# Kernel optimization log

Measured on AMD Instinct MI355X. Metric: run time of the kernel, lower is better.

## Reference

```python
import jax, jax.numpy as jnp
import numpy as np

OMEGA = 30.0
B = 65536
NUM_FREQ = 8  # int(base_dim / in_features) = 32 / 4


def _siren_w(k, out_dim, in_dim, first=False):
    bound = (1.0 / in_dim) if first else (np.sqrt(6.0 / in_dim) / OMEGA)
    return jax.random.uniform(k, (out_dim, in_dim), jnp.float32, -bound, bound)


def _lin_w(k, out_dim, in_dim):
    bound = np.sqrt(1.0 / in_dim)
    return jax.random.uniform(k, (out_dim, in_dim), jnp.float32, -bound, bound)


def setup_inputs() -> dict:
    key = jax.random.key(0)
    ks = jax.random.split(key, 16)
    E = 7
    d = {}
    d['x'] = jax.random.uniform(ks[0], (B, 4), jnp.float32, -1.0, 1.0)
    # encoder: pos_dim=64 -> sine1(128) -> sine2(256) -> resblock(256, bottleneck 128)
    d['enc_s1_w'] = _siren_w(ks[1], 128, 64, first=True); d['enc_s1_b'] = jnp.zeros((128,), jnp.float32)
    d['enc_s2_w'] = _siren_w(ks[2], 256, 128); d['enc_s2_b'] = jnp.zeros((256,), jnp.float32)
    d['res_fc1_w'] = _lin_w(ks[3], 128, 256); d['res_fc1_b'] = jnp.zeros((128,), jnp.float32)
    d['res_fc2_w'] = _lin_w(ks[4], 128, 128); d['res_fc2_b'] = jnp.zeros((128,), jnp.float32)
    d['res_fc3_w'] = _lin_w(ks[5], 256, 128); d['res_fc3_b'] = jnp.zeros((256,), jnp.float32)
    # policy: 4 -> 128 (first sine) -> 128 (sine); gate in = 256+128=384 -> 7
    d['pol_s1_w'] = _siren_w(ks[6], 128, 4, first=True); d['pol_s1_b'] = jnp.zeros((128,), jnp.float32)
    d['pol_s2_w'] = _siren_w(ks[7], 128, 128); d['pol_s2_b'] = jnp.zeros((128,), jnp.float32)
    d['gate_w'] = _siren_w(ks[8], 7, 384); d['gate_b'] = jnp.zeros((7,), jnp.float32)
    # 7 experts: SirenMLP 256 -> 256 (first sine) -> 256 (sine) -> final Linear 256 -> 1
    bnd1 = 1.0 / 256.0
    d['exp_s1_w'] = jax.random.uniform(ks[9], (E, 256, 256), jnp.float32, -bnd1, bnd1)
    d['exp_s1_b'] = jnp.zeros((E, 256), jnp.float32)
    bnd2 = np.sqrt(6.0 / 256.0) / OMEGA
    d['exp_s2_w'] = jax.random.uniform(ks[10], (E, 256, 256), jnp.float32, -bnd2, bnd2)
    d['exp_s2_b'] = jnp.zeros((E, 256), jnp.float32)
    d['exp_fin_w'] = jax.random.uniform(ks[11], (E, 1, 256), jnp.float32, -bnd2, bnd2)
    d['exp_fin_b'] = jnp.zeros((E, 1), jnp.float32)
    return d


def reference(x, enc_s1_w, enc_s1_b, enc_s2_w, enc_s2_b, res_fc1_w, res_fc1_b,
              res_fc2_w, res_fc2_b, res_fc3_w, res_fc3_b, pol_s1_w, pol_s1_b,
              pol_s2_w, pol_s2_b, gate_w, gate_b, exp_s1_w, exp_s1_b,
              exp_s2_w, exp_s2_b, exp_fin_w, exp_fin_b):
    # NeRF-style positional encoding: log-sampled freqs, no include_input
    freqs = (2.0 ** jnp.arange(NUM_FREQ, dtype=jnp.float32)) * jnp.pi  # [F]
    ang = x[:, :, None] * freqs                                        # [B,4,F]
    pe = jnp.concatenate([jnp.sin(ang), jnp.cos(ang)], axis=-1)        # [B,4,2F]
    pe = pe.reshape(x.shape[0], -1)                                    # [B,64]
    # shared encoder: sine1 -> sine2 -> bottleneck res block
    h = jnp.sin(OMEGA * (pe @ enc_s1_w.T + enc_s1_b))                  # [B,128]
    h = jnp.sin(OMEGA * (h @ enc_s2_w.T + enc_s2_b))                   # [B,256]
    r = jax.nn.relu(h @ res_fc1_w.T + res_fc1_b)                       # [B,128]
    r = jax.nn.relu(r @ res_fc2_w.T + res_fc2_b)                       # [B,128]
    r = r @ res_fc3_w.T + res_fc3_b                                    # [B,256]
    enc_feat = jax.nn.relu(r + h)                                      # [B,256]
    # policy: sine feature net + gate over [enc_feat, pol_feat]
    pf = jnp.sin(OMEGA * (x @ pol_s1_w.T + pol_s1_b))                  # [B,128]
    pf = jnp.sin(OMEGA * (pf @ pol_s2_w.T + pol_s2_b))                 # [B,128]
    logits = jnp.concatenate([enc_feat, pf], axis=-1) @ gate_w.T + gate_b  # [B,7]
    probs = jax.nn.softmax(logits, axis=-1)                            # [B,7]
    # all 7 expert SIREN MLPs as batched GEMMs over expert axis e
    e = jnp.sin(OMEGA * (jnp.einsum('bd,eod->beo', enc_feat, exp_s1_w) + exp_s1_b))  # [B,7,256]
    e = jnp.sin(OMEGA * (jnp.einsum('beh,eoh->beo', e, exp_s2_w) + exp_s2_b))        # [B,7,256]
    preds = jnp.einsum('beh,eoh->beo', e, exp_fin_w) + exp_fin_b                     # [B,7,1]
    # soft routing: probability-weighted combination
    y = jnp.sum(preds * probs[:, :, None], axis=1)                     # [B,1]
    return y
```

## Files before the change

kernel.cpp:

```cpp
#include <hip/hip_runtime.h>


typedef short v8s __attribute__((ext_vector_type(8)));
typedef float v4f __attribute__((ext_vector_type(4)));

#define KSIN 4.774648293f
#define AST 264
#define PST 9
#define N_CVT 8

__device__ __forceinline__ float bf2f(unsigned short h) {
  union { unsigned u; float f; } v; v.u = ((unsigned)h) << 16; return v.f;
}
__device__ __forceinline__ unsigned short f2bf(float f) {
  union { float f; unsigned u; } v; v.f = f;
  unsigned r = v.u + 0x7fffu + ((v.u >> 16) & 1u);
  return (unsigned short)(r >> 16);
}
__device__ __forceinline__ unsigned pack2(float a, float b) {
  return (unsigned)f2bf(a) | ((unsigned)f2bf(b) << 16);
}
__device__ __forceinline__ float sin_rev(float x) {
  return __builtin_amdgcn_sinf(x);
}
__device__ __forceinline__ float cos_rev(float x) {
  return __builtin_amdgcn_cosf(x);
}

struct CvtArgs {
  const float* src[N_CVT];
  unsigned     off[N_CVT];
  unsigned     n[N_CVT];
  float        scl[N_CVT];
};

__global__ void convert_kernel(CvtArgs a, unsigned short* __restrict__ dst) {
  const int tid = blockIdx.x * blockDim.x + threadIdx.x;
  const int stride = gridDim.x * blockDim.x;
  for (int k = 0; k < N_CVT; k++) {
    const unsigned n4 = a.n[k] >> 2;
    const float4* s = (const float4*)a.src[k];
    const float sc = a.scl[k];
    uint2* d = (uint2*)(dst + a.off[k]);
    for (unsigned i = tid; i < n4; i += stride) {
      float4 v = s[i];
      uint2 o; o.x = pack2(v.x * sc, v.y * sc); o.y = pack2(v.z * sc, v.w * sc);
      d[i] = o;
    }
    for (unsigned i = (n4 << 2) + tid; i < a.n[k]; i += stride)
      dst[a.off[k] + i] = f2bf(a.src[k][i] * sc);
  }
}

template<int K, int NPW, int ACT>
__device__ __forceinline__ void wgemm2(const unsigned short* A0,
                                       const unsigned short* A1,
                                       unsigned short* O0, unsigned short* O1,
                                       int oc,
                                       const unsigned short* __restrict__ W,
                                       const float* __restrict__ bias,
                                       const unsigned short* skip0,
                                       const unsigned short* skip1) {
  const int lane = threadIdx.x & 63;
  const int wave = threadIdx.x >> 6;
  const int m15  = lane & 15;
  const int q    = lane >> 4;
  const int n0   = wave * (NPW * 16);
  v4f acc[2][NPW][4];
#pragma unroll
  for (int tl = 0; tl < 2; tl++)
#pragma unroll
    for (int i = 0; i < NPW; i++)
#pragma unroll
      for (int j = 0; j < 4; j++) acc[tl][i][j] = (v4f){0.f, 0.f, 0.f, 0.f};

#pragma unroll
  for (int k0 = 0; k0 < K / 32; ++k0) {
    v8s b[NPW], a0[4], a1[4];
#pragma unroll
    for (int ct = 0; ct < NPW; ct++)
      b[ct] = *(const v8s*)(W + (size_t)(n0 + ct * 16 + m15) * K + k0 * 32 + q * 8);
#pragma unroll
    for (int rt = 0; rt < 4; rt++) {
      a0[rt] = *(const v8s*)(A0 + (rt * 16 + m15) * AST + k0 * 32 + q * 8);
      a1[rt] = *(const v8s*)(A1 + (rt * 16 + m15) * AST + k0 * 32 + q * 8);
    }
#pragma unroll
    for (int ct = 0; ct < NPW; ct++)
#pragma unroll
      for (int rt = 0; rt < 4; rt++) {
        acc[0][ct][rt] = __builtin_amdgcn_mfma_f32_16x16x32_bf16(b[ct], a0[rt], acc[0][ct][rt], 0, 0, 0);
        acc[1][ct][rt] = __builtin_amdgcn_mfma_f32_16x16x32_bf16(b[ct], a1[rt], acc[1][ct][rt], 0, 0, 0);
      }
  }

#pragma unroll
  for (int ct = 0; ct < NPW; ct++) {
    const int c0 = n0 + ct * 16 + q * 4;
    v4f bv = *(const v4f*)(bias + c0);
    if (ACT == 0) bv *= KSIN;
#pragma unroll
    for (int rt = 0; rt < 4; rt++) {
      const int row = rt * 16 + m15;
#pragma unroll
      for (int tl = 0; tl < 2; tl++) {
        const v4f av = acc[tl][ct][rt];
        unsigned short* OUT = tl ? O1 : O0;
        const unsigned short* skip = tl ? skip1 : skip0;
        float o0, o1, o2, o3;
        if (ACT == 2) {
          const uint2 sk = *(const uint2*)(skip + row * AST + c0);
          o0 = fmaxf(av[0] + bv[0] + bf2f((unsigned short)(sk.x & 0xffffu)), 0.f);
          o1 = fmaxf(av[1] + bv[1] + bf2f((unsigned short)(sk.x >> 16)), 0.f);
          o2 = fmaxf(av[2] + bv[2] + bf2f((unsigned short)(sk.y & 0xffffu)), 0.f);
          o3 = fmaxf(av[3] + bv[3] + bf2f((unsigned short)(sk.y >> 16)), 0.f);
        } else if (ACT == 1) {
          o0 = fmaxf(av[0] + bv[0], 0.f);
          o1 = fmaxf(av[1] + bv[1], 0.f);
          o2 = fmaxf(av[2] + bv[2], 0.f);
          o3 = fmaxf(av[3] + bv[3], 0.f);
        } else {
          o0 = sin_rev(av[0] + bv[0]);
          o1 = sin_rev(av[1] + bv[1]);
          o2 = sin_rev(av[2] + bv[2]);
          o3 = sin_rev(av[3] + bv[3]);
        }
        uint2 w2; w2.x = pack2(o0, o1); w2.y = pack2(o2, o3);
        *(uint2*)(OUT + row * AST + oc + c0) = w2;
      }
    }
  }
}

__device__ __forceinline__ void e1_mfma(const unsigned short* A0,
                                        const unsigned short* A1,
                                        const unsigned short* __restrict__ W,
                                        v4f (&acc)[2][2][4]) {
  const int lane = threadIdx.x & 63;
  const int wave = threadIdx.x >> 6;
  const int m15  = lane & 15;
  const int q    = lane >> 4;
  const int n0   = wave * 32;
#pragma unroll
  for (int tl = 0; tl < 2; tl++)
#pragma unroll
    for (int i = 0; i < 2; i++)
#pragma unroll
      for (int j = 0; j < 4; j++) acc[tl][i][j] = (v4f){0.f, 0.f, 0.f, 0.f};

#pragma unroll
  for (int k0 = 0; k0 < 8; ++k0) {
    v8s b[2], a0[4], a1[4];
#pragma unroll
    for (int ct = 0; ct < 2; ct++)
      b[ct] = *(const v8s*)(W + (size_t)(n0 + ct * 16 + m15) * 256 + k0 * 32 + q * 8);
#pragma unroll
    for (int rt = 0; rt < 4; rt++) {
      a0[rt] = *(const v8s*)(A0 + (rt * 16 + m15) * AST + k0 * 32 + q * 8);
      a1[rt] = *(const v8s*)(A1 + (rt * 16 + m15) * AST + k0 * 32 + q * 8);
    }
#pragma unroll
    for (int ct = 0; ct < 2; ct++)
#pragma unroll
      for (int rt = 0; rt < 4; rt++) {
        acc[0][ct][rt] = __builtin_amdgcn_mfma_f32_16x16x32_bf16(b[ct], a0[rt], acc[0][ct][rt], 0, 0, 0);
        acc[1][ct][rt] = __builtin_amdgcn_mfma_f32_16x16x32_bf16(b[ct], a1[rt], acc[1][ct][rt], 0, 0, 0);
      }
  }
}

__device__ __forceinline__ void e1_epi(const v4f (&acc)[2][2][4],
                                       const float* __restrict__ bias,
                                       unsigned short* O0, unsigned short* O1) {
  const int lane = threadIdx.x & 63;
  const int wave = threadIdx.x >> 6;
  const int m15  = lane & 15;
  const int q    = lane >> 4;
  const int n0   = wave * 32;
#pragma unroll
  for (int ct = 0; ct < 2; ct++) {
    const int c0 = n0 + ct * 16 + q * 4;
    v4f bv = *(const v4f*)(bias + c0);
    bv *= KSIN;
#pragma unroll
    for (int rt = 0; rt < 4; rt++) {
      const int row = rt * 16 + m15;
#pragma unroll
      for (int tl = 0; tl < 2; tl++) {
        const v4f av = acc[tl][ct][rt];
        unsigned short* OUT = tl ? O1 : O0;
        float o0 = sin_rev(av[0] + bv[0]);
        float o1 = sin_rev(av[1] + bv[1]);
        float o2 = sin_rev(av[2] + bv[2]);
        float o3 = sin_rev(av[3] + bv[3]);
        uint2 w2; w2.x = pack2(o0, o1); w2.y = pack2(o2, o3);
        *(uint2*)(OUT + row * AST + c0) = w2;
      }
    }
  }
}

__device__ __forceinline__ void wexpert2d(const unsigned short* A0,
                                          const unsigned short* A1,
                                          const unsigned short* __restrict__ W,
                                          const float* __restrict__ bias,
                                          const float* __restrict__ wfin,
                                          float* __restrict__ pp0,
                                          float* __restrict__ pp1) {
  const int lane = threadIdx.x & 63;
  const int wave = threadIdx.x >> 6;
  const int m15  = lane & 15;
  const int q    = lane >> 4;
  const int n0   = wave * 32;
  v4f acc[2][2][4];
#pragma unroll
  for (int tl = 0; tl < 2; tl++)
#pragma unroll
    for (int i = 0; i < 2; i++)
#pragma unroll
      for (int j = 0; j < 4; j++) acc[tl][i][j] = (v4f){0.f, 0.f, 0.f, 0.f};

#pragma unroll
  for (int k0 = 0; k0 < 8; ++k0) {
    v8s b[2], a0[4], a1[4];
#pragma unroll
    for (int ct = 0; ct < 2; ct++)
      b[ct] = *(const v8s*)(W + (size_t)(n0 + ct * 16 + m15) * 256 + k0 * 32 + q * 8);
#pragma unroll
    for (int rt = 0; rt < 4; rt++) {
      a0[rt] = *(const v8s*)(A0 + (rt * 16 + m15) * AST + k0 * 32 + q * 8);
      a1[rt] = *(const v8s*)(A1 + (rt * 16 + m15) * AST + k0 * 32 + q * 8);
    }
#pragma unroll
    for (int ct = 0; ct < 2; ct++)
#pragma unroll
      for (int rt = 0; rt < 4; rt++) {
        acc[0][ct][rt] = __builtin_amdgcn_mfma_f32_16x16x32_bf16(b[ct], a0[rt], acc[0][ct][rt], 0, 0, 0);
        acc[1][ct][rt] = __builtin_amdgcn_mfma_f32_16x16x32_bf16(b[ct], a1[rt], acc[1][ct][rt], 0, 0, 0);
      }
  }

  float p0[4] = {0.f, 0.f, 0.f, 0.f};
  float p1[4] = {0.f, 0.f, 0.f, 0.f};
#pragma unroll
  for (int ct = 0; ct < 2; ct++) {
    const int c0 = n0 + ct * 16 + q * 4;
    v4f bv = *(const v4f*)(bias + c0);
    bv *= KSIN;
    const v4f wf = *(const v4f*)(wfin + c0);
#pragma unroll
    for (int rt = 0; rt < 4; rt++)
#pragma unroll
      for (int r = 0; r < 4; r++) {
        p0[rt] += sin_rev(acc[0][ct][rt][r] + bv[r]) * wf[r];
        p1[rt] += sin_rev(acc[1][ct][rt][r] + bv[r]) * wf[r];
      }
  }
#pragma unroll
  for (int rt = 0; rt < 4; rt++) {
    float v0 = p0[rt], v1 = p1[rt];
    v0 += __shfl_xor(v0, 16);
    v0 += __shfl_xor(v0, 32);
    v1 += __shfl_xor(v1, 16);
    v1 += __shfl_xor(v1, 32);
    if (q == 0) {
      pp0[wave * 64 + rt * 16 + m15] = v0;
      pp1[wave * 64 + rt * 16 + m15] = v1;
    }
  }
}

__global__ __launch_bounds__(512, 2) void moe_inr_kernel(
    const float* __restrict__ x,
    const unsigned short* __restrict__ es1w, const float* __restrict__ es1b,
    const unsigned short* __restrict__ es2w, const float* __restrict__ es2b,
    const unsigned short* __restrict__ rf1w, const float* __restrict__ rf1b,
    const unsigned short* __restrict__ rf2w, const float* __restrict__ rf2b,
    const unsigned short* __restrict__ rf3w, const float* __restrict__ rf3b,
    const float* __restrict__ ps1w,          const float* __restrict__ ps1b,
    const unsigned short* __restrict__ ps2w, const float* __restrict__ ps2b,
    const float* __restrict__ gw,            const float* __restrict__ gb,
    const unsigned short* __restrict__ xs1w, const float* __restrict__ xs1b,
    const unsigned short* __restrict__ xs2w, const float* __restrict__ xs2b,
    const float* __restrict__ xfw,           const float* __restrict__ xfb,
    float* __restrict__ out) {
  __shared__ __align__(16) unsigned short P[2][64 * AST];
  __shared__ __align__(16) unsigned short Q[2][64 * AST];
  __shared__ float probs[2][64 * PST];
  __shared__ float pred_part[2][8 * 64];

  const int t   = threadIdx.x;
  const int r0g = blockIdx.x * 128;

#pragma unroll
  for (int tl = 0; tl < 2; ++tl) {
    const int row = t & 63, g = t >> 6, c = g & 3, jh = g >> 2;
    const float xv = x[(r0g + tl * 64 + row) * 4 + c];
    float sn[4], cs[4];
#pragma unroll
    for (int jj = 0; jj < 4; jj++) {
      const int j = jh * 4 + jj;
      const float rev = xv * (0.5f * (float)(1 << j));
      sn[jj] = sin_rev(rev);
      cs[jj] = cos_rev(rev);
    }
    uint2 ws; ws.x = pack2(sn[0], sn[1]); ws.y = pack2(sn[2], sn[3]);
    uint2 wc2; wc2.x = pack2(cs[0], cs[1]); wc2.y = pack2(cs[2], cs[3]);
    *(uint2*)(P[tl] + row * AST + c * 16 + jh * 4) = ws;
    *(uint2*)(P[tl] + row * AST + c * 16 + 8 + jh * 4) = wc2;
  }
  __syncthreads();
  wgemm2<64, 1, 0>(P[0], P[1], P[0], P[1], 64, es1w, es1b, nullptr, nullptr);
  __syncthreads();
  wgemm2<128, 2, 0>(P[0] + 64, P[1] + 64, Q[0], Q[1], 0, es2w, es2b, nullptr, nullptr);
  __syncthreads();
  wgemm2<256, 1, 1>(Q[0], Q[1], P[0], P[1], 0, rf1w, rf1b, nullptr, nullptr);
  __syncthreads();
  wgemm2<128, 1, 1>(P[0], P[1], P[0], P[1], 128, rf2w, rf2b, nullptr, nullptr);
  __syncthreads();
  wgemm2<128, 2, 2>(P[0] + 128, P[1] + 128, Q[0], Q[1], 0, rf3w, rf3b, Q[0], Q[1]);
  __syncthreads();
#pragma unroll
  for (int tl = 0; tl < 2; ++tl) {
    const int row = t & 63, g = t >> 6;
    const v4f xv = *(const v4f*)(x + (r0g + tl * 64 + row) * 4);
#pragma unroll
    for (int ii = 0; ii < 4; ii++) {
      float oo[4];
#pragma unroll
      for (int i2 = 0; i2 < 4; i2++) {
        const int o = g * 16 + ii * 4 + i2;
        const v4f w4 = *(const v4f*)(ps1w + o * 4);
        const float z = xv[0] * w4[0] + xv[1] * w4[1] + xv[2] * w4[2] +
                        xv[3] * w4[3] + ps1b[o];
        oo[i2] = sin_rev(KSIN * z);
      }
      uint2 w2; w2.x = pack2(oo[0], oo[1]); w2.y = pack2(oo[2], oo[3]);
      *(uint2*)(P[tl] + row * AST + g * 16 + ii * 4) = w2;
    }
  }
  __syncthreads();
  wgemm2<128, 1, 0>(P[0], P[1], P[0], P[1], 128, ps2w, ps2b, nullptr, nullptr);
  __syncthreads();
#pragma unroll
  for (int tl = 0; tl < 2; ++tl) {
    const int row = t >> 3, pp = t & 7;
    float lg[7] = {0.f, 0.f, 0.f, 0.f, 0.f, 0.f, 0.f};
#pragma unroll
    for (int u = 0; u < 6; u++) {
      const int kk = pp * 48 + u * 8;
      const v8s av = (kk < 256) ? *(const v8s*)(Q[tl] + row * AST + kk)
                                : *(const v8s*)(P[tl] + row * AST + 128 + (kk - 256));
      float af[8];
#pragma unroll
      for (int e2 = 0; e2 < 8; e2++) af[e2] = bf2f((unsigned short)av[e2]);
#pragma unroll
      for (int j = 0; j < 7; j++) {
        const v4f g0 = *(const v4f*)(gw + j * 384 + kk);
        const v4f g1 = *(const v4f*)(gw + j * 384 + kk + 4);
        lg[j] += af[0] * g0[0] + af[1] * g0[1] + af[2] * g0[2] + af[3] * g0[3] +
                 af[4] * g1[0] + af[5] * g1[1] + af[6] * g1[2] + af[7] * g1[3];
      }
    }
#pragma unroll
    for (int j = 0; j < 7; j++) {
      float s = lg[j];
      s += __shfl_xor(s, 1);
      s += __shfl_xor(s, 2);
      s += __shfl_xor(s, 4);
      lg[j] = s;
    }
    if (pp == 0) {
#pragma unroll
      for (int j = 0; j < 7; j++) probs[tl][row * PST + j] = lg[j] + gb[j];
    }
  }
  __syncthreads();
  float yr = 0.f;
  v4f acc1[2][2][4];
  e1_mfma(Q[0], Q[1], xs1w, acc1);
  if (t < 128) {
    const int tl = t >> 6, row = t & 63;
    float m = probs[tl][row * PST];
#pragma unroll
    for (int j = 1; j < 7; j++) m = fmaxf(m, probs[tl][row * PST + j]);
    float s = 0.f, e[7];
#pragma unroll
    for (int j = 0; j < 7; j++) { e[j] = __expf(probs[tl][row * PST + j] - m); s += e[j]; }
    const float inv = 1.f / s;
#pragma unroll
    for (int j = 0; j < 7; j++) probs[tl][row * PST + j] = e[j] * inv;
  }
  e1_epi(acc1, xs1b, P[0], P[1]);
  __syncthreads();
  for (int ex = 0; ex < 7; ++ex) {
    wexpert2d(P[0], P[1], xs2w + ex * 65536, xs2b + ex * 256, xfw + ex * 256,
              pred_part[0], pred_part[1]);
    if (ex < 6) e1_mfma(Q[0], Q[1], xs1w + (ex + 1) * 65536, acc1);
    __syncthreads();
    if (ex < 6) e1_epi(acc1, xs1b + (ex + 1) * 256, P[0], P[1]);
    if (t < 128) {
      const int tl = t >> 6, row = t & 63;
      float pr = 0.f;
#pragma unroll
      for (int w = 0; w < 8; w++) pr += pred_part[tl][w * 64 + row];
      yr += (pr + xfb[ex]) * probs[tl][row * PST + ex];
    }
    if (ex < 6) __syncthreads();
  }
  if (t < 128) out[r0g + t] = yr;
}

extern "C" void kernel_launch(void* const* d_in, const int* in_sizes, int n_in,
                              void* d_out, int out_size, void* d_ws, size_t ws_size,
                              hipStream_t stream) {
  (void)out_size; (void)n_in; (void)ws_size;
  const int   idx[N_CVT] = {1, 3, 5, 7, 9, 13, 17, 19};
  const float scl[N_CVT] = {KSIN, KSIN, 1.f, 1.f, 1.f, KSIN, KSIN, KSIN};
  unsigned off[N_CVT], cur = 0;
  CvtArgs a;
  for (int i = 0; i < N_CVT; i++) {
    off[i] = cur;
    a.src[i] = (const float*)d_in[idx[i]];
    a.off[i] = cur;
    a.n[i]   = (unsigned)in_sizes[idx[i]];
    a.scl[i] = scl[i];
    cur += ((unsigned)in_sizes[idx[i]] + 7u) & ~7u;
  }
  unsigned short* dst = (unsigned short*)d_ws;
  hipLaunchKernelGGL(convert_kernel, dim3(1024), dim3(256), 0, stream, a, dst);
  hipLaunchKernelGGL(moe_inr_kernel, dim3(65536 / 128), dim3(512), 0, stream,
      (const float*)d_in[0],
      dst + off[0], (const float*)d_in[2],
      dst + off[1], (const float*)d_in[4],
      dst + off[2], (const float*)d_in[6],
      dst + off[3], (const float*)d_in[8],
      dst + off[4], (const float*)d_in[10],
      (const float*)d_in[11], (const float*)d_in[12],
      dst + off[5], (const float*)d_in[14],
      (const float*)d_in[15], (const float*)d_in[16],
      dst + off[6], (const float*)d_in[18],
      dst + off[7], (const float*)d_in[20],
      (const float*)d_in[21], (const float*)d_in[22],
      (float*)d_out);
}
```

Baseline: 320.9 us.

## Prefetch next expert's second-layer weights into registers during current expert GEMM

The expert loop now loads the next expert's second-layer weight fragments into a register buffer while the current expert's MFMAs run, hiding global-memory latency behind compute. The first expert's weights are prefetched before the loop. A barrier after the residual fc3 GEMM is removed, on the view that the following policy layer writes only to shared-memory columns that fc3 does not read. The weight-conversion kernel's grid is also shrunk. The prefetch buffer adds about 64 VGPRs per thread, which risks spills or lower occupancy. The last iteration issues a redundant reload of expert 6's weights.

```diff
diff --git a/kernel.cpp b/kernel.cpp
--- a/kernel.cpp
+++ b/kernel.cpp
@@ -132,6 +132,20 @@
   }
 }
 
+__device__ __forceinline__ void e2_prefetch(const unsigned short* __restrict__ W,
+                                            v8s (&bpf)[2][8]) {
+  const int lane = threadIdx.x & 63;
+  const int wave = threadIdx.x >> 6;
+  const int m15  = lane & 15;
+  const int q    = lane >> 4;
+  const int n0   = wave * 32;
+#pragma unroll
+  for (int k0 = 0; k0 < 8; k0++)
+#pragma unroll
+    for (int ct = 0; ct < 2; ct++)
+      bpf[ct][k0] = *(const v8s*)(W + (size_t)(n0 + ct * 16 + m15) * 256 + k0 * 32 + q * 8);
+}
+
 __device__ __forceinline__ void e1_mfma(const unsigned short* A0,
                                         const unsigned short* A1,
                                         const unsigned short* __restrict__ W,
@@ -200,9 +214,10 @@
   }
 }
 
-__device__ __forceinline__ void wexpert2d(const unsigned short* A0,
+__device__ __forceinline__ void wexpert2p(const unsigned short* A0,
                                           const unsigned short* A1,
-                                          const unsigned short* __restrict__ W,
+                                          v8s (&bpf)[2][8],
+                                          const unsigned short* __restrict__ Wnext,
                                           const float* __restrict__ bias,
                                           const float* __restrict__ wfin,
                                           float* __restrict__ pp0,
@@ -222,22 +237,23 @@
 
 #pragma unroll
   for (int k0 = 0; k0 < 8; ++k0) {
-    v8s b[2], a0[4], a1[4];
-#pragma unroll
-    for (int ct = 0; ct < 2; ct++)
-      b[ct] = *(const v8s*)(W + (size_t)(n0 + ct * 16 + m15) * 256 + k0 * 32 + q * 8);
+    v8s a0[4], a1[4];
 #pragma unroll
     for (int rt = 0; rt < 4; rt++) {
       a0[rt] = *(const v8s*)(A0 + (rt * 16 + m15) * AST + k0 * 32 + q * 8);
       a1[rt] = *(const v8s*)(A1 + (rt * 16 + m15) * AST + k0 * 32 + q * 8);
     }
-#pragma unroll
-    for (int ct = 0; ct < 2; ct++)
-#pragma unroll
-      for (int rt = 0; rt < 4; rt++) {
-        acc[0][ct][rt] = __builtin_amdgcn_mfma_f32_16x16x32_bf16(b[ct], a0[rt], acc[0][ct][rt], 0, 0, 0);
-        acc[1][ct][rt] = __builtin_amdgcn_mfma_f32_16x16x32_bf16(b[ct], a1[rt], acc[1][ct][rt], 0, 0, 0);
-      }
+    const v8s b0 = bpf[0][k0];
+    const v8s b1 = bpf[1][k0];
+    bpf[0][k0] = *(const v8s*)(Wnext + (size_t)(n0 + m15) * 256 + k0 * 32 + q * 8);
+    bpf[1][k0] = *(const v8s*)(Wnext + (size_t)(n0 + 16 + m15) * 256 + k0 * 32 + q * 8);
+#pragma unroll
+    for (int rt = 0; rt < 4; rt++) {
+      acc[0][0][rt] = __builtin_amdgcn_mfma_f32_16x16x32_bf16(b0, a0[rt], acc[0][0][rt], 0, 0, 0);
+      acc[1][0][rt] = __builtin_amdgcn_mfma_f32_16x16x32_bf16(b0, a1[rt], acc[1][0][rt], 0, 0, 0);
+      acc[0][1][rt] = __builtin_amdgcn_mfma_f32_16x16x32_bf16(b1, a0[rt], acc[0][1][rt], 0, 0, 0);
+      acc[1][1][rt] = __builtin_amdgcn_mfma_f32_16x16x32_bf16(b1, a1[rt], acc[1][1][rt], 0, 0, 0);
+    }
   }
 
   float p0[4] = {0.f, 0.f, 0.f, 0.f};
@@ -319,7 +335,6 @@
   wgemm2<128, 1, 1>(P[0], P[1], P[0], P[1], 128, rf2w, rf2b, nullptr, nullptr);
   __syncthreads();
   wgemm2<128, 2, 2>(P[0] + 128, P[1] + 128, Q[0], Q[1], 0, rf3w, rf3b, Q[0], Q[1]);
-  __syncthreads();
 #pragma unroll
   for (int tl = 0; tl < 2; ++tl) {
     const int row = t & 63, g = t >> 6;
@@ -378,7 +393,9 @@
   __syncthreads();
   float yr = 0.f;
   v4f acc1[2][2][4];
+  v8s bpf[2][8];
   e1_mfma(Q[0], Q[1], xs1w, acc1);
+  e2_prefetch(xs2w, bpf);
   if (t < 128) {
     const int tl = t >> 6, row = t & 63;
     float m = probs[tl][row * PST];
@@ -394,8 +411,9 @@
   e1_epi(acc1, xs1b, P[0], P[1]);
   __syncthreads();
   for (int ex = 0; ex < 7; ++ex) {
-    wexpert2d(P[0], P[1], xs2w + ex * 65536, xs2b + ex * 256, xfw + ex * 256,
-              pred_part[0], pred_part[1]);
+    const int nxt = (ex < 6) ? ex + 1 : 6;
+    wexpert2p(P[0], P[1], bpf, xs2w + nxt * 65536,
+              xs2b + ex * 256, xfw + ex * 256, pred_part[0], pred_part[1]);
     if (ex < 6) e1_mfma(Q[0], Q[1], xs1w + (ex + 1) * 65536, acc1);
     __syncthreads();
     if (ex < 6) e1_epi(acc1, xs1b + (ex + 1) * 256, P[0], P[1]);
@@ -428,7 +446,7 @@
     cur += ((unsigned)in_sizes[idx[i]] + 7u) & ~7u;
   }
   unsigned short* dst = (unsigned short*)d_ws;
-  hipLaunchKernelGGL(convert_kernel, dim3(1024), dim3(256), 0, stream, a, dst);
+  hipLaunchKernelGGL(convert_kernel, dim3(256), dim3(256), 0, stream, a, dst);
   hipLaunchKernelGGL(moe_inr_kernel, dim3(65536 / 128), dim3(512), 0, stream,
       (const float*)d_in[0],
       dst + off[0], (const float*)d_in[2],
```

Measured after the change: 342.5 us. 6.7% more time.
